# Performance work log

Hardware: AMD Instinct MI355X
Metric: run time of the kernel (lower is better)

Reference implementation:

```python
import jax, jax.numpy as jnp
import numpy as np

HIDDEN = 1024
N_HEADS = 16
HEAD = HIDDEN // N_HEADS  # 64
DFF = 4 * HIDDEN


def setup_inputs() -> dict:
    key = jax.random.key(0)
    ks = jax.random.split(key, 12)
    B, T = 4, 2048
    s = 0.02
    return {
        "x": jax.random.normal(ks[0], (B, T, HIDDEN), jnp.float32),
        # per-head QKV weights, stacked: [H, HIDDEN, HEAD] (no bias, as in Head)
        "Wq": jax.random.normal(ks[1], (N_HEADS, HIDDEN, HEAD), jnp.float32) * s,
        "Wk": jax.random.normal(ks[2], (N_HEADS, HIDDEN, HEAD), jnp.float32) * s,
        "Wv": jax.random.normal(ks[3], (N_HEADS, HIDDEN, HEAD), jnp.float32) * s,
        "Wo": jax.random.normal(ks[4], (HIDDEN, HIDDEN), jnp.float32) * s,
        "bo": jnp.zeros((HIDDEN,), jnp.float32),
        "W1": jax.random.normal(ks[5], (HIDDEN, DFF), jnp.float32) * s,
        "b1": jnp.zeros((DFF,), jnp.float32),
        "W2": jax.random.normal(ks[6], (DFF, HIDDEN), jnp.float32) * s,
        "b2": jnp.zeros((HIDDEN,), jnp.float32),
        "g1": jnp.ones((HIDDEN,), jnp.float32),
        "be1": jnp.zeros((HIDDEN,), jnp.float32),
        "g2": jnp.ones((HIDDEN,), jnp.float32),
        "be2": jnp.zeros((HIDDEN,), jnp.float32),
    }


def _layernorm(x, g, b, eps=1e-5):
    mu = jnp.mean(x, axis=-1, keepdims=True)
    var = jnp.mean(jnp.square(x - mu), axis=-1, keepdims=True)
    return (x - mu) * jax.lax.rsqrt(var + eps) * g + b


def _attention(h, Wq, Wk, Wv, Wo, bo):
    B, T, C = h.shape
    # [B,T,C] x [H,C,D] -> [B,H,T,D]
    Q = jnp.einsum('btc,hcd->bhtd', h, Wq)
    K = jnp.einsum('btc,hcd->bhtd', h, Wk)
    V = jnp.einsum('btc,hcd->bhtd', h, Wv)
    scores = jnp.einsum('bhtd,bhsd->bhts', Q, K) / np.sqrt(HEAD).astype(np.float32)
    causal = jnp.tril(jnp.ones((T, T), bool))
    scores = jnp.where(causal, scores, -jnp.inf)
    attn = jax.nn.softmax(scores, axis=-1)
    out = jnp.einsum('bhts,bhsd->bhtd', attn, V)
    # concat heads in order (head axis -> last dim blocks)
    out = out.transpose(0, 2, 1, 3).reshape(B, T, C)
    return out @ Wo + bo


def reference(x, Wq, Wk, Wv, Wo, bo, W1, b1, W2, b2, g1, be1, g2, be2):
    x = x + _attention(_layernorm(x, g1, be1), Wq, Wk, Wv, Wo, bo)
    h = _layernorm(x, g2, be2)
    ff = jax.nn.relu(h @ W1 + b1) @ W2 + b2
    return x + ff
```

## Files before the change

kernel.cpp:

```cpp
#include <hip/hip_runtime.h>
#include <hip/hip_bf16.h>
#include <stdint.h>


#define HID 1024
#define NH 16
#define HD 64
#define DFF 4096
#define BATCH 4
#define SEQ 2048
#define NTOK (BATCH*SEQ)

typedef unsigned short u16;
typedef unsigned int u32;
typedef __attribute__((ext_vector_type(4))) float f32x4;
typedef __attribute__((ext_vector_type(16))) float f32x16;
typedef __attribute__((ext_vector_type(8))) __bf16 bf16x8;

__device__ __forceinline__ u16 f2bf(float f) {
    unsigned int u = __float_as_uint(f);
    u = (u + 0x7fffu + ((u >> 16) & 1u)) >> 16;
    return (u16)u;
}

__device__ __forceinline__ u32 cvtpk(float lo, float hi) {
    u32 d;
    asm("v_cvt_pk_bf16_f32 %0, %1, %2" : "=v"(d) : "v"(lo), "v"(hi));
    return d;
}

__device__ __forceinline__ void plswap(u32& a, u32& b) {
    asm volatile("v_permlane32_swap_b32 %0, %1" : "+v"(a), "+v"(b));
}

__device__ __forceinline__ void gload_lds16(const void* g, void* lds) {
    __builtin_amdgcn_global_load_lds(
        (const __attribute__((address_space(1))) unsigned int*)(uintptr_t)g,
        (__attribute__((address_space(3))) unsigned int*)(uintptr_t)lds, 16, 0, 0);
}

template <int N>
__device__ __forceinline__ void waitvm() {
    if constexpr (N == 8)      asm volatile("s_waitcnt vmcnt(8)" ::: "memory");
    else if constexpr (N == 6) asm volatile("s_waitcnt vmcnt(6)" ::: "memory");
    else if constexpr (N == 4) asm volatile("s_waitcnt vmcnt(4)" ::: "memory");
    else if constexpr (N == 3) asm volatile("s_waitcnt vmcnt(3)" ::: "memory");
    else                       asm volatile("s_waitcnt vmcnt(0)" ::: "memory");
}

__device__ __forceinline__ void pipe_barrier() {
    __builtin_amdgcn_sched_barrier(0);
    __builtin_amdgcn_s_barrier();
    __builtin_amdgcn_sched_barrier(0);
}

__global__ __launch_bounds__(256) void ln_kernel(const float* __restrict__ x,
                                                 const float* __restrict__ g,
                                                 const float* __restrict__ be,
                                                 u16* __restrict__ out) {
    __shared__ float red[10];
    const int row = blockIdx.x, tid = threadIdx.x;
    const float4 v = ((const float4*)(x + (size_t)row * HID))[tid];
    float s  = v.x + v.y + v.z + v.w;
    float s2 = v.x*v.x + v.y*v.y + v.z*v.z + v.w*v.w;
    for (int off = 32; off > 0; off >>= 1) {
        s  += __shfl_down(s, off, 64);
        s2 += __shfl_down(s2, off, 64);
    }
    if ((tid & 63) == 0) { red[tid >> 6] = s; red[4 + (tid >> 6)] = s2; }
    __syncthreads();
    if (tid == 0) {
        red[8] = red[0] + red[1] + red[2] + red[3];
        red[9] = red[4] + red[5] + red[6] + red[7];
    }
    __syncthreads();
    const float mu  = red[8] * (1.f / HID);
    const float var = red[9] * (1.f / HID) - mu * mu;
    const float rstd = rsqrtf(var + 1e-5f);
    const float4 g4 = ((const float4*)g)[tid];
    const float4 b4 = ((const float4*)be)[tid];
    ushort4 o;
    o.x = f2bf((v.x - mu) * rstd * g4.x + b4.x);
    o.y = f2bf((v.y - mu) * rstd * g4.y + b4.y);
    o.z = f2bf((v.z - mu) * rstd * g4.z + b4.z);
    o.w = f2bf((v.w - mu) * rstd * g4.w + b4.w);
    ((ushort4*)(out + (size_t)row * HID))[tid] = o;
}

__global__ __launch_bounds__(256) void transpose_w(const float* __restrict__ in,
                                                   u16* __restrict__ out, int R, int C) {
    __shared__ float t[32][33];
    const int r0 = blockIdx.x * 32, c0 = blockIdx.y * 32;
    const float* inb = in + (size_t)blockIdx.z * R * C;
    u16* outb = out + (size_t)blockIdx.z * R * C;
    const int tid = threadIdx.x;
    const int tr = tid >> 3, tc = (tid & 7) * 4;
    const float4 v = *(const float4*)&inb[(size_t)(r0 + tr) * C + c0 + tc];
    t[tr][tc] = v.x; t[tr][tc + 1] = v.y; t[tr][tc + 2] = v.z; t[tr][tc + 3] = v.w;
    __syncthreads();
    ushort4 o;
    o.x = f2bf(t[tc + 0][tr]);
    o.y = f2bf(t[tc + 1][tr]);
    o.z = f2bf(t[tc + 2][tr]);
    o.w = f2bf(t[tc + 3][tr]);
    *(ushort4*)&outb[(size_t)(c0 + tr) * R + r0 + tc] = o;
}

__global__ __launch_bounds__(256) void transpose_v(const u16* __restrict__ in,
                                                   u16* __restrict__ out) {
    __shared__ u16 t[64][65];
    const int s0 = blockIdx.x * 64;
    const size_t bh = blockIdx.y;
    const u16* inb = in + bh * SEQ * HD;
    u16* outb = out + bh * HD * SEQ;
    const int tid = threadIdx.x;
    const int r = tid >> 2, c = (tid & 3) * 16;
    bf16x8 a = *(const bf16x8*)&inb[(size_t)(s0 + r) * HD + c];
    bf16x8 b = *(const bf16x8*)&inb[(size_t)(s0 + r) * HD + c + 8];
    #pragma unroll
    for (int i = 0; i < 8; i++) {
        t[r][c + i]     = ((const u16*)&a)[i];
        t[r][c + 8 + i] = ((const u16*)&b)[i];
    }
    __syncthreads();
    u16 o0[8], o1[8];
    #pragma unroll
    for (int i = 0; i < 8; i++) { o0[i] = t[c + i][r]; o1[i] = t[c + 8 + i][r]; }
    *(bf16x8*)&outb[(size_t)r * SEQ + s0 + c]     = *(const bf16x8*)o0;
    *(bf16x8*)&outb[(size_t)r * SEQ + s0 + c + 8] = *(const bf16x8*)o1;
}

template <int BN, int MODE>
__global__ __launch_bounds__(512, 2) void gemm_p(const u16* __restrict__ A,
                                                 const u16* __restrict__ B,
                                                 float* __restrict__ outf,
                                                 u16* __restrict__ outh,
                                                 const float* __restrict__ bias,
                                                 const float* __restrict__ resid,
                                                 int K, int N) {
    constexpr int ASL = 16384;
    constexpr int BSL = (BN == 256) ? 16384 : 8192;
    constexpr int BRD = (BN == 256) ? 2 : 1;
    constexpr int LPS = 2 + BRD;
    constexpr int WN  = (BN == 256) ? 4 : 2;
    constexpr int MR  = (BN == 256) ? 128 : 64;
    constexpr int MF  = MR / 16;
    __shared__ char lds[4 * ASL + 4 * BSL];
    char* const ldsB = lds + 4 * ASL;

    const int tid = threadIdx.x;
    const int w = tid >> 6, l = tid & 63;
    const int l15 = l & 15, lg = l >> 4;
    const int wr = w / WN, wc = w % WN;
    const int m0 = (blockIdx.x & 31) * 256;
    const int n0 = (blockIdx.x >> 5) * BN;
    const size_t Kb = (size_t)K * 2;
    const int H = K >> 5;

    int gar[2], gac[2], gbr[BRD], gbc[BRD];
    #pragma unroll
    for (int rd = 0; rd < 2; ++rd) {
        const int p = rd * 8192 + tid * 16;
        const int line = p >> 7, s16 = (p >> 4) & 7;
        const int u = (s16 * 16) ^ ((line & 7) << 4);
        gar[rd] = line + ((u >> 6) & 1) * 128;
        gac[rd] = u & 63;
    }
    #pragma unroll
    for (int rd = 0; rd < BRD; ++rd) {
        const int p = rd * 8192 + tid * 16;
        const int line = p >> 7, s16 = (p >> 4) & 7;
        const int u = (s16 * 16) ^ ((line & 7) << 4);
        gbr[rd] = line + ((u >> 6) & 1) * ((BN == 256) ? 128 : 64);
        gbc[rd] = u & 63;
    }

    const char* Ag = (const char*)A + (size_t)m0 * Kb;
    const char* Bg = (const char*)B + (size_t)n0 * Kb;

    auto stage = [&](int h) {
        const int slot = h & 3;
        const size_t kby = (size_t)h * 64;
        #pragma unroll
        for (int rd = 0; rd < 2; ++rd)
            gload_lds16(Ag + (size_t)gar[rd] * Kb + kby + gac[rd],
                        lds + slot * ASL + rd * 8192 + w * 1024);
        #pragma unroll
        for (int rd = 0; rd < BRD; ++rd)
            gload_lds16(Bg + (size_t)gbr[rd] * Kb + kby + gbc[rd],
                        ldsB + slot * BSL + rd * 8192 + w * 1024);
    };

    int offA[MF], offB[4];
    #pragma unroll
    for (int mi = 0; mi < MF; ++mi) {
        const int row = wr * MR + mi * 16 + l15;
        offA[mi] = (row & 127) * 128 + ((((row >> 7) * 64) + lg * 16) ^ ((l15 & 7) << 4));
    }
    #pragma unroll
    for (int nj = 0; nj < 4; ++nj) {
        const int row = wc * 64 + nj * 16 + l15;
        if (BN == 256)
            offB[nj] = (row & 127) * 128 + ((((row >> 7) * 64) + lg * 16) ^ ((l15 & 7) << 4));
        else
            offB[nj] = (row & 63) * 128 + ((((row >> 6) * 64) + lg * 16) ^ ((l15 & 7) << 4));
    }

    f32x4 acc[MF][4] = {};

    auto compute = [&](int hh) {
        const char* la = lds + (hh & 3) * ASL;
        const char* lb = ldsB + (hh & 3) * BSL;
        bf16x8 af[MF], bf[4];
        #pragma unroll
        for (int mi = 0; mi < MF; ++mi) af[mi] = *(const bf16x8*)(la + offA[mi]);
        #pragma unroll
        for (int nj = 0; nj < 4; ++nj) bf[nj] = *(const bf16x8*)(lb + offB[nj]);
        __builtin_amdgcn_s_setprio(1);
        #pragma unroll
        for (int mi = 0; mi < MF; ++mi)
            #pragma unroll
            for (int nj = 0; nj < 4; ++nj)
                acc[mi][nj] = __builtin_amdgcn_mfma_f32_16x16x32_bf16(af[mi], bf[nj], acc[mi][nj], 0, 0, 0);
        __builtin_amdgcn_s_setprio(0);
    };

    stage(0); stage(1); stage(2);
    waitvm<2 * LPS>();
    pipe_barrier();

    int h = 0;
    for (; h < H - 3; ++h) {
        compute(h);
        stage(h + 3);
        waitvm<2 * LPS>();
        pipe_barrier();
    }
    compute(h); waitvm<LPS>(); pipe_barrier(); ++h;
    compute(h); waitvm<0>();   pipe_barrier(); ++h;
    compute(h);

    const int r00 = m0 + wr * MR + (lg << 2);
    const int c00 = n0 + wc * 64 + l15;
    #pragma unroll
    for (int nj = 0; nj < 4; ++nj) {
        const int c = c00 + nj * 16;
        if (MODE == 0) {
            const int which = c >> 10, hc = c & 1023;
            const int hh = hc >> 6, d = hc & 63;
            const float sc2 = (which == 0) ? 0.125f : 1.0f;
            u16* outp = outh + (size_t)which * ((size_t)NTOK * HID);
            #pragma unroll
            for (int mi = 0; mi < MF; ++mi)
                #pragma unroll
                for (int j = 0; j < 4; ++j) {
                    const int r = r00 + mi * 16 + j;
                    const int b = r >> 11, t = r & (SEQ - 1);
                    outp[((size_t)(b * NH + hh) * SEQ + t) * HD + d] = f2bf(acc[mi][nj][j] * sc2);
                }
        } else if (MODE == 1) {
            const float bi = bias[c];
            #pragma unroll
            for (int mi = 0; mi < MF; ++mi)
                #pragma unroll
                for (int j = 0; j < 4; ++j) {
                    const int r = r00 + mi * 16 + j;
                    const size_t idx = (size_t)r * N + c;
                    outf[idx] = resid[idx] + acc[mi][nj][j] + bi;
                }
        } else {
            const float bi = bias[c];
            #pragma unroll
            for (int mi = 0; mi < MF; ++mi)
                #pragma unroll
                for (int j = 0; j < 4; ++j) {
                    const int r = r00 + mi * 16 + j;
                    const float v = acc[mi][nj][j] + bi;
                    outh[(size_t)r * N + c] = f2bf(v > 0.f ? v : 0.f);
                }
        }
    }
}

__global__ __launch_bounds__(256) void attn_kernel(const u16* __restrict__ Q,
                                                   const u16* __restrict__ K,
                                                   const u16* __restrict__ Vt,
                                                   u16* __restrict__ O) {
    __shared__ u16 Kl[2][64 * 64];
    __shared__ u16 Vl[2][64 * 64];
    const int qt = (gridDim.x - 1) - blockIdx.x;
    const int bh = blockIdx.y;
    const int tid = threadIdx.x, w = tid >> 6, l = tid & 63;
    const int q32 = l & 31, hi = l >> 5;
    const int qbase = qt * 128 + w * 32;
    const int qrow = qbase + q32;

    const u16* Qg = Q + ((size_t)bh * SEQ + qrow) * HD;
    bf16x8 qf[4];
    #pragma unroll
    for (int c = 0; c < 4; ++c)
        qf[c] = *(const bf16x8*)&Qg[c * 16 + hi * 8];

    f32x16 oa[2] = {};
    float m = -1e30f, lsum = 0.f;

    const u16* Kg0 = K + (size_t)bh * SEQ * HD;
    const u16* Vg0 = Vt + (size_t)bh * HD * SEQ;
    const int sr8 = tid >> 3;
    const int sc8 = (tid & 7) * 16;

    bf16x8 kreg[2], vreg[2];
    auto load_tile = [&](int st) {
        const char* Kg = (const char*)(Kg0 + (size_t)st * 64 * HD);
        const char* Vg = (const char*)(Vg0 + st * 64);
        #pragma unroll
        for (int it = 0; it < 2; it++) {
            kreg[it] = *(const bf16x8*)(Kg + (size_t)(it * 32 + sr8) * 128 + sc8);
            vreg[it] = *(const bf16x8*)(Vg + (size_t)(it * 32 + sr8) * (SEQ * 2) + sc8);
        }
    };
    auto write_tile = [&](int buf) {
        char* KlB = (char*)Kl[buf];
        char* VlB = (char*)Vl[buf];
        const int sw = (sr8 & 7) << 4;
        #pragma unroll
        for (int it = 0; it < 2; it++) {
            *(bf16x8*)(KlB + (it * 32 + sr8) * 128 + (sc8 ^ sw)) = kreg[it];
            *(bf16x8*)(VlB + (it * 32 + sr8) * 128 + (sc8 ^ sw)) = vreg[it];
        }
    };

    const int ntiles = 2 * qt + 2;
    const int tlast = (qbase + 31) >> 6;

    load_tile(0);
    write_tile(0);

    for (int st = 0; st < ntiles; ++st) {
        const int cur = st & 1;
        __syncthreads();
        const bool pf = (st + 1 < ntiles);
        if (pf) load_tile(st + 1);

        if (st <= tlast) {
            const char* KlB = (const char*)Kl[cur];
            const char* VlB = (const char*)Vl[cur];

            f32x16 s[2];
            __builtin_amdgcn_s_setprio(1);
            #pragma unroll
            for (int a = 0; a < 2; ++a) {
                const int row = a * 32 + q32;
                const char* base = KlB + row * 128;
                const int sw = (row & 7) << 4;
                f32x16 accs = {};
                #pragma unroll
                for (int ds4 = 0; ds4 < 4; ++ds4) {
                    bf16x8 kf = *(const bf16x8*)(base + ((ds4 * 32 + hi * 16) ^ sw));
                    accs = __builtin_amdgcn_mfma_f32_32x32x16_bf16(kf, qf[ds4], accs, 0, 0, 0);
                }
                s[a] = accs;
            }
            __builtin_amdgcn_s_setprio(0);

            if (st == tlast) {
                const int st64 = st * 64;
                #pragma unroll
                for (int a = 0; a < 2; ++a)
                    #pragma unroll
                    for (int r = 0; r < 16; ++r) {
                        const int kvg = st64 + a * 32 + (r & 3) + 8 * (r >> 2) + 4 * hi;
                        if (kvg > qrow) s[a][r] = -1e30f;
                    }
            }

            float pm0 = -1e30f, pm1 = -1e30f, pm2 = -1e30f, pm3 = -1e30f;
            #pragma unroll
            for (int r = 0; r < 16; r += 4) {
                pm0 = fmaxf(pm0, fmaxf(s[0][r + 0], s[1][r + 0]));
                pm1 = fmaxf(pm1, fmaxf(s[0][r + 1], s[1][r + 1]));
                pm2 = fmaxf(pm2, fmaxf(s[0][r + 2], s[1][r + 2]));
                pm3 = fmaxf(pm3, fmaxf(s[0][r + 3], s[1][r + 3]));
            }
            float pmax = fmaxf(fmaxf(pm0, pm1), fmaxf(pm2, pm3));
            pmax = fmaxf(pmax, __shfl_xor(pmax, 32, 64));

            if (!__all(pmax <= m + 8.f)) {
                const float newm = fmaxf(m, pmax);
                const float sc = __expf(m - newm);
                m = newm;
                lsum *= sc;
                #pragma unroll
                for (int d = 0; d < 2; ++d)
                    #pragma unroll
                    for (int r = 0; r < 16; ++r)
                        oa[d][r] *= sc;
            }

            float s0 = 0.f, s1 = 0.f, s2 = 0.f, s3 = 0.f;
            #pragma unroll
            for (int a = 0; a < 2; ++a)
                #pragma unroll
                for (int r = 0; r < 16; r += 4) {
                    float p0 = __expf(s[a][r + 0] - m);
                    float p1 = __expf(s[a][r + 1] - m);
                    float p2 = __expf(s[a][r + 2] - m);
                    float p3 = __expf(s[a][r + 3] - m);
                    s[a][r + 0] = p0; s[a][r + 1] = p1;
                    s[a][r + 2] = p2; s[a][r + 3] = p3;
                    s0 += p0; s1 += p1; s2 += p2; s3 += p3;
                }
            float psum = (s0 + s1) + (s2 + s3);
            psum += __shfl_xor(psum, 32, 64);
            lsum += psum;

            u32 W[2][4][2];
            #pragma unroll
            for (int a = 0; a < 2; ++a)
                #pragma unroll
                for (int i = 0; i < 4; ++i) {
                    W[a][i][0] = cvtpk(s[a][4 * i + 0], s[a][4 * i + 1]);
                    W[a][i][1] = cvtpk(s[a][4 * i + 2], s[a][4 * i + 3]);
                }
            bf16x8 pa[4];
            #pragma unroll
            for (int a = 0; a < 2; ++a)
                #pragma unroll
                for (int j = 0; j < 2; ++j) {
                    u32 a0 = W[a][2 * j][0], b0 = W[a][2 * j + 1][0];
                    u32 a1 = W[a][2 * j][1], b1 = W[a][2 * j + 1][1];
                    plswap(a0, b0);
                    plswap(a1, b1);
                    union { u32 ww[4]; bf16x8 v; } u_;
                    u_.ww[0] = a0; u_.ww[1] = a1; u_.ww[2] = b0; u_.ww[3] = b1;
                    pa[2 * a + j] = u_.v;
                }

            __builtin_amdgcn_s_setprio(1);
            #pragma unroll
            for (int dblk = 0; dblk < 2; ++dblk) {
                const int row = dblk * 32 + q32;
                const char* base = VlB + row * 128;
                const int sw = (row & 7) << 4;
                #pragma unroll
                for (int s4 = 0; s4 < 4; ++s4) {
                    bf16x8 vf = *(const bf16x8*)(base + ((s4 * 32 + hi * 16) ^ sw));
                    oa[dblk] = __builtin_amdgcn_mfma_f32_32x32x16_bf16(vf, pa[s4], oa[dblk], 0, 0, 0);
                }
            }
            __builtin_amdgcn_s_setprio(0);
        }

        if (pf) write_tile(cur ^ 1);
    }

    const int b = bh >> 4, h = bh & 15;
    const float inv = 1.f / lsum;
    u16* Orow = O + ((size_t)b * SEQ + qrow) * HID + h * HD;
    #pragma unroll
    for (int dblk = 0; dblk < 2; ++dblk)
        #pragma unroll
        for (int i = 0; i < 4; ++i) {
            ushort4 st4;
            st4.x = f2bf(oa[dblk][4 * i + 0] * inv);
            st4.y = f2bf(oa[dblk][4 * i + 1] * inv);
            st4.z = f2bf(oa[dblk][4 * i + 2] * inv);
            st4.w = f2bf(oa[dblk][4 * i + 3] * inv);
            *(ushort4*)&Orow[dblk * 32 + 8 * i + 4 * hi] = st4;
        }
}

extern "C" void kernel_launch(void* const* d_in, const int* in_sizes, int n_in,
                              void* d_out, int out_size, void* d_ws, size_t ws_size,
                              hipStream_t stream) {
    (void)in_sizes; (void)n_in; (void)out_size; (void)ws_size;
    const float* x   = (const float*)d_in[0];
    const float* Wq  = (const float*)d_in[1];
    const float* Wk  = (const float*)d_in[2];
    const float* Wv  = (const float*)d_in[3];
    const float* Wo  = (const float*)d_in[4];
    const float* bo  = (const float*)d_in[5];
    const float* W1  = (const float*)d_in[6];
    const float* b1  = (const float*)d_in[7];
    const float* W2  = (const float*)d_in[8];
    const float* b2  = (const float*)d_in[9];
    const float* g1  = (const float*)d_in[10];
    const float* be1 = (const float*)d_in[11];
    const float* g2  = (const float*)d_in[12];
    const float* be2 = (const float*)d_in[13];
    float* out = (float*)d_out;

    char* ws = (char*)d_ws;
    size_t off = 0;
    auto alloc = [&](size_t bytes) { void* p = ws + off; off += bytes; return p; };
    u16* Wqkv_t = (u16*)alloc((size_t)3 * HID * HID * 2);
    u16* Wo_t = (u16*)alloc((size_t)HID * HID * 2);
    u16* W1_t = (u16*)alloc((size_t)DFF * HID * 2);
    u16* W2_t = (u16*)alloc((size_t)HID * DFF * 2);
    u16* h1   = (u16*)alloc((size_t)NTOK * HID * 2);
    u16* Qb   = (u16*)alloc((size_t)NTOK * HID * 2);
    u16* Kb   = (u16*)alloc((size_t)NTOK * HID * 2);
    u16* Vb   = (u16*)alloc((size_t)NTOK * HID * 2);
    u16* Vt   = (u16*)alloc((size_t)NTOK * HID * 2);
    float* x2 = (float*)alloc((size_t)NTOK * HID * 4);
    u16* ff1  = Qb;

    transpose_w<<<dim3(32, 2, 16), 256, 0, stream>>>(Wq, Wqkv_t, HID, HD);
    transpose_w<<<dim3(32, 2, 16), 256, 0, stream>>>(Wk, Wqkv_t + (size_t)HID * HID, HID, HD);
    transpose_w<<<dim3(32, 2, 16), 256, 0, stream>>>(Wv, Wqkv_t + (size_t)2 * HID * HID, HID, HD);
    transpose_w<<<dim3(32, 32, 1), 256, 0, stream>>>(Wo, Wo_t, HID, HID);
    transpose_w<<<dim3(32, 128, 1), 256, 0, stream>>>(W1, W1_t, HID, DFF);
    transpose_w<<<dim3(128, 32, 1), 256, 0, stream>>>(W2, W2_t, DFF, HID);

    ln_kernel<<<NTOK, 256, 0, stream>>>(x, g1, be1, h1);

    gemm_p<128, 0><<<dim3(32 * 24), 512, 0, stream>>>(h1, Wqkv_t, nullptr, Qb,
                                                      nullptr, nullptr, HID, 3072);

    transpose_v<<<dim3(SEQ / 64, BATCH * NH), 256, 0, stream>>>(Vb, Vt);

    u16* attn_out = Vb;
    attn_kernel<<<dim3(SEQ / 128, BATCH * NH), 256, 0, stream>>>(Qb, Kb, Vt, attn_out);

    gemm_p<128, 1><<<dim3(32 * 8), 512, 0, stream>>>(attn_out, Wo_t, x2, nullptr, bo, x, HID, HID);

    ln_kernel<<<NTOK, 256, 0, stream>>>(x2, g2, be2, h1);

    gemm_p<256, 2><<<dim3(32 * 16), 512, 0, stream>>>(h1, W1_t, nullptr, ff1, b1, nullptr, HID, DFF);

    gemm_p<128, 1><<<dim3(32 * 8), 512, 0, stream>>>(ff1, W2_t, out, nullptr, b2, x2, DFF, HID);
}
```

Measured before the change: 561.2 us.

## Rework GEMM tiling, pipeline depth, block swizzle and pair causal attention tiles

Replaces the GEMM with a wave-count-parameterised version. Every wave now owns a 128x64 tile, the pipeline uses three LDS stages instead of four, block indices are remapped across groups of eight for locality, and the Wo/W2 GEMMs drop to 256-thread blocks. The attention kernel now has each block handle a short and a long causal query tile in sequence, which balances work across blocks and halves the grid. Together these aim to raise per-wave reuse and even out the load, at the cost of more registers per wave, a shallower prefetch and fewer blocks to hide latency.

```diff
diff --git a/kernel.cpp b/kernel.cpp
--- a/kernel.cpp
+++ b/kernel.cpp
@@ -41,10 +41,8 @@
 
 template <int N>
 __device__ __forceinline__ void waitvm() {
-    if constexpr (N == 8)      asm volatile("s_waitcnt vmcnt(8)" ::: "memory");
-    else if constexpr (N == 6) asm volatile("s_waitcnt vmcnt(6)" ::: "memory");
+    if constexpr (N == 6)      asm volatile("s_waitcnt vmcnt(6)" ::: "memory");
     else if constexpr (N == 4) asm volatile("s_waitcnt vmcnt(4)" ::: "memory");
-    else if constexpr (N == 3) asm volatile("s_waitcnt vmcnt(3)" ::: "memory");
     else                       asm volatile("s_waitcnt vmcnt(0)" ::: "memory");
 }
 
@@ -130,37 +128,42 @@
     *(bf16x8*)&outb[(size_t)r * SEQ + s0 + c + 8] = *(const bf16x8*)o1;
 }
 
-template <int BN, int MODE>
-__global__ __launch_bounds__(512, 2) void gemm_p(const u16* __restrict__ A,
-                                                 const u16* __restrict__ B,
-                                                 float* __restrict__ outf,
-                                                 u16* __restrict__ outh,
-                                                 const float* __restrict__ bias,
-                                                 const float* __restrict__ resid,
-                                                 int K, int N) {
+template <int WAVES, int MODE>
+__global__ __launch_bounds__(WAVES * 64, 2) void gemm6(const u16* __restrict__ A,
+                                                       const u16* __restrict__ B,
+                                                       float* __restrict__ outf,
+                                                       u16* __restrict__ outh,
+                                                       const float* __restrict__ bias,
+                                                       const float* __restrict__ resid,
+                                                       int K, int N) {
+    constexpr int THREADS = WAVES * 64;
+    constexpr int WN  = WAVES / 2;
+    constexpr int BN  = WN * 64;
     constexpr int ASL = 16384;
-    constexpr int BSL = (BN == 256) ? 16384 : 8192;
-    constexpr int BRD = (BN == 256) ? 2 : 1;
-    constexpr int LPS = 2 + BRD;
-    constexpr int WN  = (BN == 256) ? 4 : 2;
-    constexpr int MR  = (BN == 256) ? 128 : 64;
-    constexpr int MF  = MR / 16;
-    __shared__ char lds[4 * ASL + 4 * BSL];
-    char* const ldsB = lds + 4 * ASL;
+    constexpr int BSL = BN * 64;
+    constexpr int ARD = ASL / (THREADS * 16);
+    constexpr int BRD = BSL / (THREADS * 16);
+    constexpr int LPS = ARD + BRD;
+    constexpr int LB  = BSL >> 7;
+    __shared__ char lds[3 * (ASL + BSL)];
+    char* const ldsB = lds + 3 * ASL;
 
     const int tid = threadIdx.x;
     const int w = tid >> 6, l = tid & 63;
     const int l15 = l & 15, lg = l >> 4;
     const int wr = w / WN, wc = w % WN;
-    const int m0 = (blockIdx.x & 31) * 256;
-    const int n0 = (blockIdx.x >> 5) * BN;
+
+    const int nwg = gridDim.x;
+    const int wg = (blockIdx.x & 7) * (nwg >> 3) + (blockIdx.x >> 3);
+    const int m0 = (wg & 31) * 256;
+    const int n0 = (wg >> 5) * BN;
     const size_t Kb = (size_t)K * 2;
     const int H = K >> 5;
 
-    int gar[2], gac[2], gbr[BRD], gbc[BRD];
-    #pragma unroll
-    for (int rd = 0; rd < 2; ++rd) {
-        const int p = rd * 8192 + tid * 16;
+    int gar[ARD], gac[ARD], gbr[BRD], gbc[BRD];
+    #pragma unroll
+    for (int rd = 0; rd < ARD; ++rd) {
+        const int p = rd * (THREADS * 16) + tid * 16;
         const int line = p >> 7, s16 = (p >> 4) & 7;
         const int u = (s16 * 16) ^ ((line & 7) << 4);
         gar[rd] = line + ((u >> 6) & 1) * 128;
@@ -168,79 +171,80 @@
     }
     #pragma unroll
     for (int rd = 0; rd < BRD; ++rd) {
-        const int p = rd * 8192 + tid * 16;
+        const int p = rd * (THREADS * 16) + tid * 16;
         const int line = p >> 7, s16 = (p >> 4) & 7;
         const int u = (s16 * 16) ^ ((line & 7) << 4);
-        gbr[rd] = line + ((u >> 6) & 1) * ((BN == 256) ? 128 : 64);
+        gbr[rd] = line + ((u >> 6) & 1) * LB;
         gbc[rd] = u & 63;
     }
 
     const char* Ag = (const char*)A + (size_t)m0 * Kb;
     const char* Bg = (const char*)B + (size_t)n0 * Kb;
 
-    auto stage = [&](int h) {
-        const int slot = h & 3;
-        const size_t kby = (size_t)h * 64;
-        #pragma unroll
-        for (int rd = 0; rd < 2; ++rd)
+    auto stage = [&](int h, int slot) {
+        const size_t kby = (size_t)h << 6;
+        #pragma unroll
+        for (int rd = 0; rd < ARD; ++rd)
             gload_lds16(Ag + (size_t)gar[rd] * Kb + kby + gac[rd],
-                        lds + slot * ASL + rd * 8192 + w * 1024);
+                        lds + slot * ASL + rd * (THREADS * 16) + w * 1024);
         #pragma unroll
         for (int rd = 0; rd < BRD; ++rd)
             gload_lds16(Bg + (size_t)gbr[rd] * Kb + kby + gbc[rd],
-                        ldsB + slot * BSL + rd * 8192 + w * 1024);
+                        ldsB + slot * BSL + rd * (THREADS * 16) + w * 1024);
     };
 
-    int offA[MF], offB[4];
-    #pragma unroll
-    for (int mi = 0; mi < MF; ++mi) {
-        const int row = wr * MR + mi * 16 + l15;
-        offA[mi] = (row & 127) * 128 + ((((row >> 7) * 64) + lg * 16) ^ ((l15 & 7) << 4));
+    int offA[8], offB[4];
+    #pragma unroll
+    for (int mi = 0; mi < 8; ++mi) {
+        const int row = wr * 128 + mi * 16 + l15;
+        offA[mi] = (row & 127) * 128 + ((((row >> 7) * 64) + lg * 16) ^ ((row & 7) << 4));
     }
     #pragma unroll
     for (int nj = 0; nj < 4; ++nj) {
         const int row = wc * 64 + nj * 16 + l15;
-        if (BN == 256)
-            offB[nj] = (row & 127) * 128 + ((((row >> 7) * 64) + lg * 16) ^ ((l15 & 7) << 4));
-        else
-            offB[nj] = (row & 63) * 128 + ((((row >> 6) * 64) + lg * 16) ^ ((l15 & 7) << 4));
-    }
-
-    f32x4 acc[MF][4] = {};
-
-    auto compute = [&](int hh) {
-        const char* la = lds + (hh & 3) * ASL;
-        const char* lb = ldsB + (hh & 3) * BSL;
-        bf16x8 af[MF], bf[4];
-        #pragma unroll
-        for (int mi = 0; mi < MF; ++mi) af[mi] = *(const bf16x8*)(la + offA[mi]);
+        offB[nj] = (row & (LB - 1)) * 128 +
+                   ((((row / LB) * 64) + lg * 16) ^ ((row & 7) << 4));
+    }
+
+    f32x4 acc[8][4] = {};
+
+    auto compute = [&](int hh, int slot) {
+        const char* la = lds + slot * ASL;
+        const char* lb = ldsB + slot * BSL;
+        bf16x8 af[8], bf[4];
+        #pragma unroll
+        for (int mi = 0; mi < 8; ++mi) af[mi] = *(const bf16x8*)(la + offA[mi]);
         #pragma unroll
         for (int nj = 0; nj < 4; ++nj) bf[nj] = *(const bf16x8*)(lb + offB[nj]);
         __builtin_amdgcn_s_setprio(1);
         #pragma unroll
-        for (int mi = 0; mi < MF; ++mi)
+        for (int mi = 0; mi < 8; ++mi)
             #pragma unroll
             for (int nj = 0; nj < 4; ++nj)
                 acc[mi][nj] = __builtin_amdgcn_mfma_f32_16x16x32_bf16(af[mi], bf[nj], acc[mi][nj], 0, 0, 0);
         __builtin_amdgcn_s_setprio(0);
     };
 
-    stage(0); stage(1); stage(2);
-    waitvm<2 * LPS>();
+    stage(0, 0); stage(1, 1);
+    waitvm<LPS>();
     pipe_barrier();
 
-    int h = 0;
-    for (; h < H - 3; ++h) {
-        compute(h);
-        stage(h + 3);
-        waitvm<2 * LPS>();
+    int cur = 0, nx2 = 2;
+    for (int h = 0; h < H - 2; ++h) {
+        compute(h, cur);
+        stage(h + 2, nx2);
+        waitvm<LPS>();
         pipe_barrier();
-    }
-    compute(h); waitvm<LPS>(); pipe_barrier(); ++h;
-    compute(h); waitvm<0>();   pipe_barrier(); ++h;
-    compute(h);
-
-    const int r00 = m0 + wr * MR + (lg << 2);
+        cur = (cur == 2) ? 0 : cur + 1;
+        nx2 = (nx2 == 2) ? 0 : nx2 + 1;
+    }
+    compute(H - 2, cur);
+    waitvm<0>();
+    pipe_barrier();
+    cur = (cur == 2) ? 0 : cur + 1;
+    compute(H - 1, cur);
+
+    const int r00 = m0 + wr * 128 + (lg << 2);
     const int c00 = n0 + wc * 64 + l15;
     #pragma unroll
     for (int nj = 0; nj < 4; ++nj) {
@@ -251,7 +255,7 @@
             const float sc2 = (which == 0) ? 0.125f : 1.0f;
             u16* outp = outh + (size_t)which * ((size_t)NTOK * HID);
             #pragma unroll
-            for (int mi = 0; mi < MF; ++mi)
+            for (int mi = 0; mi < 8; ++mi)
                 #pragma unroll
                 for (int j = 0; j < 4; ++j) {
                     const int r = r00 + mi * 16 + j;
@@ -261,7 +265,7 @@
         } else if (MODE == 1) {
             const float bi = bias[c];
             #pragma unroll
-            for (int mi = 0; mi < MF; ++mi)
+            for (int mi = 0; mi < 8; ++mi)
                 #pragma unroll
                 for (int j = 0; j < 4; ++j) {
                     const int r = r00 + mi * 16 + j;
@@ -271,7 +275,7 @@
         } else {
             const float bi = bias[c];
             #pragma unroll
-            for (int mi = 0; mi < MF; ++mi)
+            for (int mi = 0; mi < 8; ++mi)
                 #pragma unroll
                 for (int j = 0; j < 4; ++j) {
                     const int r = r00 + mi * 16 + j;
@@ -288,21 +292,10 @@
                                                    u16* __restrict__ O) {
     __shared__ u16 Kl[2][64 * 64];
     __shared__ u16 Vl[2][64 * 64];
-    const int qt = (gridDim.x - 1) - blockIdx.x;
+    const int kpair = blockIdx.x;
     const int bh = blockIdx.y;
     const int tid = threadIdx.x, w = tid >> 6, l = tid & 63;
     const int q32 = l & 31, hi = l >> 5;
-    const int qbase = qt * 128 + w * 32;
-    const int qrow = qbase + q32;
-
-    const u16* Qg = Q + ((size_t)bh * SEQ + qrow) * HD;
-    bf16x8 qf[4];
-    #pragma unroll
-    for (int c = 0; c < 4; ++c)
-        qf[c] = *(const bf16x8*)&Qg[c * 16 + hi * 8];
-
-    f32x16 oa[2] = {};
-    float m = -1e30f, lsum = 0.f;
 
     const u16* Kg0 = K + (size_t)bh * SEQ * HD;
     const u16* Vg0 = Vt + (size_t)bh * HD * SEQ;
@@ -330,144 +323,161 @@
         }
     };
 
-    const int ntiles = 2 * qt + 2;
-    const int tlast = (qbase + 31) >> 6;
-
-    load_tile(0);
-    write_tile(0);
-
-    for (int st = 0; st < ntiles; ++st) {
-        const int cur = st & 1;
+    for (int ph = 0; ph < 2; ++ph) {
+        const int qt = ph ? (SEQ / 128 - 1) - kpair : kpair;
+        const int qbase = qt * 128 + w * 32;
+        const int qrow = qbase + q32;
+
+        const u16* Qg = Q + ((size_t)bh * SEQ + qrow) * HD;
+        bf16x8 qf[4];
+        #pragma unroll
+        for (int c = 0; c < 4; ++c)
+            qf[c] = *(const bf16x8*)&Qg[c * 16 + hi * 8];
+
+        f32x16 oa[2] = {};
+        float m = -1e30f, lsum = 0.f;
+
+        const int ntiles = 2 * qt + 2;
+        const int tlast = (qbase + 31) >> 6;
+
+        load_tile(0);
+        write_tile(0);
+
+        for (int st = 0; st < ntiles; ++st) {
+            const int cur = st & 1;
+            __syncthreads();
+            const bool pf = (st + 1 < ntiles);
+            if (pf) load_tile(st + 1);
+
+            if (st <= tlast) {
+                const char* KlB = (const char*)Kl[cur];
+                const char* VlB = (const char*)Vl[cur];
+
+                f32x16 s[2];
+                __builtin_amdgcn_s_setprio(1);
+                #pragma unroll
+                for (int a = 0; a < 2; ++a) {
+                    const int row = a * 32 + q32;
+                    const char* base = KlB + row * 128;
+                    const int sw = (row & 7) << 4;
+                    f32x16 accs = {};
+                    #pragma unroll
+                    for (int ds4 = 0; ds4 < 4; ++ds4) {
+                        bf16x8 kf = *(const bf16x8*)(base + ((ds4 * 32 + hi * 16) ^ sw));
+                        accs = __builtin_amdgcn_mfma_f32_32x32x16_bf16(kf, qf[ds4], accs, 0, 0, 0);
+                    }
+                    s[a] = accs;
+                }
+                __builtin_amdgcn_s_setprio(0);
+
+                if (st == tlast) {
+                    const int st64 = st * 64;
+                    #pragma unroll
+                    for (int a = 0; a < 2; ++a)
+                        #pragma unroll
+                        for (int r = 0; r < 16; ++r) {
+                            const int kvg = st64 + a * 32 + (r & 3) + 8 * (r >> 2) + 4 * hi;
+                            if (kvg > qrow) s[a][r] = -1e30f;
+                        }
+                }
+
+                float pm0 = -1e30f, pm1 = -1e30f, pm2 = -1e30f, pm3 = -1e30f;
+                #pragma unroll
+                for (int r = 0; r < 16; r += 4) {
+                    pm0 = fmaxf(pm0, fmaxf(s[0][r + 0], s[1][r + 0]));
+                    pm1 = fmaxf(pm1, fmaxf(s[0][r + 1], s[1][r + 1]));
+                    pm2 = fmaxf(pm2, fmaxf(s[0][r + 2], s[1][r + 2]));
+                    pm3 = fmaxf(pm3, fmaxf(s[0][r + 3], s[1][r + 3]));
+                }
+                float pmax = fmaxf(fmaxf(pm0, pm1), fmaxf(pm2, pm3));
+                pmax = fmaxf(pmax, __shfl_xor(pmax, 32, 64));
+
+                if (!__all(pmax <= m + 8.f)) {
+                    const float newm = fmaxf(m, pmax);
+                    const float sc = __expf(m - newm);
+                    m = newm;
+                    lsum *= sc;
+                    #pragma unroll
+                    for (int d = 0; d < 2; ++d)
+                        #pragma unroll
+                        for (int r = 0; r < 16; ++r)
+                            oa[d][r] *= sc;
+                }
+
+                float s0 = 0.f, s1 = 0.f, s2 = 0.f, s3 = 0.f;
+                #pragma unroll
+                for (int a = 0; a < 2; ++a)
+                    #pragma unroll
+                    for (int r = 0; r < 16; r += 4) {
+                        float p0 = __expf(s[a][r + 0] - m);
+                        float p1 = __expf(s[a][r + 1] - m);
+                        float p2 = __expf(s[a][r + 2] - m);
+                        float p3 = __expf(s[a][r + 3] - m);
+                        s[a][r + 0] = p0; s[a][r + 1] = p1;
+                        s[a][r + 2] = p2; s[a][r + 3] = p3;
+                        s0 += p0; s1 += p1; s2 += p2; s3 += p3;
+                    }
+                float psum = (s0 + s1) + (s2 + s3);
+                psum += __shfl_xor(psum, 32, 64);
+                lsum += psum;
+
+                u32 W[2][4][2];
+                #pragma unroll
+                for (int a = 0; a < 2; ++a)
+                    #pragma unroll
+                    for (int i = 0; i < 4; ++i) {
+                        W[a][i][0] = cvtpk(s[a][4 * i + 0], s[a][4 * i + 1]);
+                        W[a][i][1] = cvtpk(s[a][4 * i + 2], s[a][4 * i + 3]);
+                    }
+                bf16x8 pa[4];
+                #pragma unroll
+                for (int a = 0; a < 2; ++a)
+                    #pragma unroll
+                    for (int j = 0; j < 2; ++j) {
+                        u32 a0 = W[a][2 * j][0], b0 = W[a][2 * j + 1][0];
+                        u32 a1 = W[a][2 * j][1], b1 = W[a][2 * j + 1][1];
+                        plswap(a0, b0);
+                        plswap(a1, b1);
+                        union { u32 ww[4]; bf16x8 v; } u_;
+                        u_.ww[0] = a0; u_.ww[1] = a1; u_.ww[2] = b0; u_.ww[3] = b1;
+                        pa[2 * a + j] = u_.v;
+                    }
+
+                __builtin_amdgcn_s_setprio(1);
+                #pragma unroll
+                for (int dblk = 0; dblk < 2; ++dblk) {
+                    const int row = dblk * 32 + q32;
+                    const char* base = VlB + row * 128;
+                    const int sw = (row & 7) << 4;
+                    #pragma unroll
+                    for (int s4 = 0; s4 < 4; ++s4) {
+                        bf16x8 vf = *(const bf16x8*)(base + ((s4 * 32 + hi * 16) ^ sw));
+                        oa[dblk] = __builtin_amdgcn_mfma_f32_32x32x16_bf16(vf, pa[s4], oa[dblk], 0, 0, 0);
+                    }
+                }
+                __builtin_amdgcn_s_setprio(0);
+            }
+
+            if (pf) write_tile(cur ^ 1);
+        }
+
+        const int b = bh >> 4, h = bh & 15;
+        const float inv = 1.f / lsum;
+        u16* Orow = O + ((size_t)b * SEQ + qrow) * HID + h * HD;
+        #pragma unroll
+        for (int dblk = 0; dblk < 2; ++dblk)
+            #pragma unroll
+            for (int i = 0; i < 4; ++i) {
+                ushort4 st4;
+                st4.x = f2bf(oa[dblk][4 * i + 0] * inv);
+                st4.y = f2bf(oa[dblk][4 * i + 1] * inv);
+                st4.z = f2bf(oa[dblk][4 * i + 2] * inv);
+                st4.w = f2bf(oa[dblk][4 * i + 3] * inv);
+                *(ushort4*)&Orow[dblk * 32 + 8 * i + 4 * hi] = st4;
+            }
+
         __syncthreads();
-        const bool pf = (st + 1 < ntiles);
-        if (pf) load_tile(st + 1);
-
-        if (st <= tlast) {
-            const char* KlB = (const char*)Kl[cur];
-            const char* VlB = (const char*)Vl[cur];
-
-            f32x16 s[2];
-            __builtin_amdgcn_s_setprio(1);
-            #pragma unroll
-            for (int a = 0; a < 2; ++a) {
-                const int row = a * 32 + q32;
-                const char* base = KlB + row * 128;
-                const int sw = (row & 7) << 4;
-                f32x16 accs = {};
-                #pragma unroll
-                for (int ds4 = 0; ds4 < 4; ++ds4) {
-                    bf16x8 kf = *(const bf16x8*)(base + ((ds4 * 32 + hi * 16) ^ sw));
-                    accs = __builtin_amdgcn_mfma_f32_32x32x16_bf16(kf, qf[ds4], accs, 0, 0, 0);
-                }
-                s[a] = accs;
-            }
-            __builtin_amdgcn_s_setprio(0);
-
-            if (st == tlast) {
-                const int st64 = st * 64;
-                #pragma unroll
-                for (int a = 0; a < 2; ++a)
-                    #pragma unroll
-                    for (int r = 0; r < 16; ++r) {
-                        const int kvg = st64 + a * 32 + (r & 3) + 8 * (r >> 2) + 4 * hi;
-                        if (kvg > qrow) s[a][r] = -1e30f;
-                    }
-            }
-
-            float pm0 = -1e30f, pm1 = -1e30f, pm2 = -1e30f, pm3 = -1e30f;
-            #pragma unroll
-            for (int r = 0; r < 16; r += 4) {
-                pm0 = fmaxf(pm0, fmaxf(s[0][r + 0], s[1][r + 0]));
-                pm1 = fmaxf(pm1, fmaxf(s[0][r + 1], s[1][r + 1]));
-                pm2 = fmaxf(pm2, fmaxf(s[0][r + 2], s[1][r + 2]));
-                pm3 = fmaxf(pm3, fmaxf(s[0][r + 3], s[1][r + 3]));
-            }
-            float pmax = fmaxf(fmaxf(pm0, pm1), fmaxf(pm2, pm3));
-            pmax = fmaxf(pmax, __shfl_xor(pmax, 32, 64));
-
-            if (!__all(pmax <= m + 8.f)) {
-                const float newm = fmaxf(m, pmax);
-                const float sc = __expf(m - newm);
-                m = newm;
-                lsum *= sc;
-                #pragma unroll
-                for (int d = 0; d < 2; ++d)
-                    #pragma unroll
-                    for (int r = 0; r < 16; ++r)
-                        oa[d][r] *= sc;
-            }
-
-            float s0 = 0.f, s1 = 0.f, s2 = 0.f, s3 = 0.f;
-            #pragma unroll
-            for (int a = 0; a < 2; ++a)
-                #pragma unroll
-                for (int r = 0; r < 16; r += 4) {
-                    float p0 = __expf(s[a][r + 0] - m);
-                    float p1 = __expf(s[a][r + 1] - m);
-                    float p2 = __expf(s[a][r + 2] - m);
-                    float p3 = __expf(s[a][r + 3] - m);
-                    s[a][r + 0] = p0; s[a][r + 1] = p1;
-                    s[a][r + 2] = p2; s[a][r + 3] = p3;
-                    s0 += p0; s1 += p1; s2 += p2; s3 += p3;
-                }
-            float psum = (s0 + s1) + (s2 + s3);
-            psum += __shfl_xor(psum, 32, 64);
-            lsum += psum;
-
-            u32 W[2][4][2];
-            #pragma unroll
-            for (int a = 0; a < 2; ++a)
-                #pragma unroll
-                for (int i = 0; i < 4; ++i) {
-                    W[a][i][0] = cvtpk(s[a][4 * i + 0], s[a][4 * i + 1]);
-                    W[a][i][1] = cvtpk(s[a][4 * i + 2], s[a][4 * i + 3]);
-                }
-            bf16x8 pa[4];
-            #pragma unroll
-            for (int a = 0; a < 2; ++a)
-                #pragma unroll
-                for (int j = 0; j < 2; ++j) {
-                    u32 a0 = W[a][2 * j][0], b0 = W[a][2 * j + 1][0];
-                    u32 a1 = W[a][2 * j][1], b1 = W[a][2 * j + 1][1];
-                    plswap(a0, b0);
-                    plswap(a1, b1);
-                    union { u32 ww[4]; bf16x8 v; } u_;
-                    u_.ww[0] = a0; u_.ww[1] = a1; u_.ww[2] = b0; u_.ww[3] = b1;
-                    pa[2 * a + j] = u_.v;
-                }
-
-            __builtin_amdgcn_s_setprio(1);
-            #pragma unroll
-            for (int dblk = 0; dblk < 2; ++dblk) {
-                const int row = dblk * 32 + q32;
-                const char* base = VlB + row * 128;
-                const int sw = (row & 7) << 4;
-                #pragma unroll
-                for (int s4 = 0; s4 < 4; ++s4) {
-                    bf16x8 vf = *(const bf16x8*)(base + ((s4 * 32 + hi * 16) ^ sw));
-                    oa[dblk] = __builtin_amdgcn_mfma_f32_32x32x16_bf16(vf, pa[s4], oa[dblk], 0, 0, 0);
-                }
-            }
-            __builtin_amdgcn_s_setprio(0);
-        }
-
-        if (pf) write_tile(cur ^ 1);
-    }
-
-    const int b = bh >> 4, h = bh & 15;
-    const float inv = 1.f / lsum;
-    u16* Orow = O + ((size_t)b * SEQ + qrow) * HID + h * HD;
-    #pragma unroll
-    for (int dblk = 0; dblk < 2; ++dblk)
-        #pragma unroll
-        for (int i = 0; i < 4; ++i) {
-            ushort4 st4;
-            st4.x = f2bf(oa[dblk][4 * i + 0] * inv);
-            st4.y = f2bf(oa[dblk][4 * i + 1] * inv);
-            st4.z = f2bf(oa[dblk][4 * i + 2] * inv);
-            st4.w = f2bf(oa[dblk][4 * i + 3] * inv);
-            *(ushort4*)&Orow[dblk * 32 + 8 * i + 4 * hi] = st4;
-        }
+    }
 }
 
 extern "C" void kernel_launch(void* const* d_in, const int* in_sizes, int n_in,
@@ -514,19 +524,19 @@
 
     ln_kernel<<<NTOK, 256, 0, stream>>>(x, g1, be1, h1);
 
-    gemm_p<128, 0><<<dim3(32 * 24), 512, 0, stream>>>(h1, Wqkv_t, nullptr, Qb,
-                                                      nullptr, nullptr, HID, 3072);
+    gemm6<8, 0><<<dim3(32 * 12), 512, 0, stream>>>(h1, Wqkv_t, nullptr, Qb,
+                                                   nullptr, nullptr, HID, 3072);
 
     transpose_v<<<dim3(SEQ / 64, BATCH * NH), 256, 0, stream>>>(Vb, Vt);
 
     u16* attn_out = Vb;
-    attn_kernel<<<dim3(SEQ / 128, BATCH * NH), 256, 0, stream>>>(Qb, Kb, Vt, attn_out);
-
-    gemm_p<128, 1><<<dim3(32 * 8), 512, 0, stream>>>(attn_out, Wo_t, x2, nullptr, bo, x, HID, HID);
+    attn_kernel<<<dim3(SEQ / 256, BATCH * NH), 256, 0, stream>>>(Qb, Kb, Vt, attn_out);
+
+    gemm6<4, 1><<<dim3(32 * 8), 256, 0, stream>>>(attn_out, Wo_t, x2, nullptr, bo, x, HID, HID);
 
     ln_kernel<<<NTOK, 256, 0, stream>>>(x2, g2, be2, h1);
 
-    gemm_p<256, 2><<<dim3(32 * 16), 512, 0, stream>>>(h1, W1_t, nullptr, ff1, b1, nullptr, HID, DFF);
-
-    gemm_p<128, 1><<<dim3(32 * 8), 512, 0, stream>>>(ff1, W2_t, out, nullptr, b2, x2, DFF, HID);
-}
+    gemm6<8, 2><<<dim3(32 * 16), 512, 0, stream>>>(h1, W1_t, nullptr, ff1, b1, nullptr, HID, DFF);
+
+    gemm6<4, 1><<<dim3(32 * 8), 256, 0, stream>>>(ff1, W2_t, out, nullptr, b2, x2, DFF, HID);
+}
```

New measurement: 580.7 us. 1.03x slower.
